# Optimization experiments

Hardware: AMD Instinct MI355X
Metric: run time of the kernel (lower is better)

The kernel has to match this reference:

```python
import jax, jax.numpy as jnp
import numpy as np
from jax import lax

EPS = 1e-5  # BatchNorm eps; eval-mode BN with running_mean=0, running_var=1


def _bn(v, g, b):
    return v * (g / jnp.sqrt(1.0 + EPS)) + b


def setup_inputs() -> dict:
    key = jax.random.key(0)
    ks = jax.random.split(key, 8)
    B, I, O, H, W, E, K, r = 16, 128, 128, 128, 128, 16, 3, 8
    Ir, Or = I // r, O // r
    f = jax.random.normal
    return {
        "x": f(ks[0], (B, I, H, W), jnp.float32),
        "experts": f(ks[1], (E, O, I, K, K), jnp.float32) * 0.05,
        "rw1": f(ks[2], (Ir, I), jnp.float32) * 0.05,
        "rbn1_g": jnp.ones((Ir,), jnp.float32),
        "rbn1_b": jnp.zeros((Ir,), jnp.float32),
        "rw2": f(ks[3], (I, Ir), jnp.float32) * 0.05,
        "rbn2_g": jnp.ones((I,), jnp.float32),
        "rbn2_b": jnp.zeros((I,), jnp.float32),
        "rw3": f(ks[4], (E, I), jnp.float32) * 0.05,
        "rb3": jnp.zeros((E,), jnp.float32),
        "ca_w1": f(ks[5], (Or, O), jnp.float32) * 0.05,
        "ca_bn1_g": jnp.ones((Or,), jnp.float32),
        "ca_bn1_b": jnp.zeros((Or,), jnp.float32),
        "ca_w2": f(ks[6], (O, Or), jnp.float32) * 0.05,
        "ca_bn2_g": jnp.ones((O,), jnp.float32),
        "ca_bn2_b": jnp.zeros((O,), jnp.float32),
        "sa_w": f(ks[7], (1, 2, 7, 7), jnp.float32) * 0.05,
        "sa_bn_g": jnp.ones((1,), jnp.float32),
        "sa_bn_b": jnp.zeros((1,), jnp.float32),
    }


def reference(x, experts, rw1, rbn1_g, rbn1_b, rw2, rbn2_g, rbn2_b, rw3, rb3,
              ca_w1, ca_bn1_g, ca_bn1_b, ca_w2, ca_bn2_g, ca_bn2_b,
              sa_w, sa_bn_g, sa_bn_b):
    B, I, H, W = x.shape
    E, O, _, K, _ = experts.shape
    # --- routing: avgpool -> 1x1 conv (matmul) -> BN -> ReLU -> 1x1 -> BN -> sigmoid -> 1x1 -> softmax
    p = jnp.mean(x, axis=(2, 3))                                  # [B, I]
    h = jax.nn.relu(_bn(p @ rw1.T, rbn1_g, rbn1_b))               # [B, I/r]
    g = jax.nn.sigmoid(_bn(h @ rw2.T, rbn2_g, rbn2_b))            # [B, I]
    rweights = jax.nn.softmax(g @ rw3.T + rb3, axis=1)            # [B, E]
    # --- expert-weighted kernel generation as a single GEMM
    w = jnp.einsum('be,eoihw->boihw', rweights, experts)          # [B, O, I, K, K]
    # --- per-sample conv via grouped conv (groups = B), stride=1, padding=1
    out = lax.conv_general_dilated(
        x.reshape(1, B * I, H, W),
        w.reshape(B * O, I, K, K),
        window_strides=(1, 1), padding=((1, 1), (1, 1)),
        dimension_numbers=('NCHW', 'OIHW', 'NCHW'),
        feature_group_count=B,
    ).reshape(B, O, H, W)
    # --- SE channel attention
    cp = jnp.mean(out, axis=(2, 3))                               # [B, O]
    ch = jax.nn.relu(_bn(cp @ ca_w1.T, ca_bn1_g, ca_bn1_b))
    cw = jax.nn.sigmoid(_bn(ch @ ca_w2.T, ca_bn2_g, ca_bn2_b))    # [B, O]
    out = out * cw[:, :, None, None]
    # --- CBAM spatial attention
    sp = jnp.concatenate([jnp.mean(out, axis=1, keepdims=True),
                          jnp.max(out, axis=1, keepdims=True)], axis=1)  # [B,2,H,W]
    sw = lax.conv_general_dilated(sp, sa_w, (1, 1), ((3, 3), (3, 3)),
                                  dimension_numbers=('NCHW', 'OIHW', 'NCHW'))
    sw = jax.nn.sigmoid(_bn(sw, sa_bn_g.reshape(1, 1, 1, 1), sa_bn_b.reshape(1, 1, 1, 1)))
    out = out * sw
    # --- residual (in_channels == out_channels -> Identity)
    return out + x
```

## Files before the change

### kernel.cpp

```cpp
#include <hip/hip_runtime.h>

typedef unsigned short ushort_t;
typedef __attribute__((ext_vector_type(4))) float float4_t;
typedef __attribute__((ext_vector_type(8))) short short8_t;
typedef __attribute__((ext_vector_type(8))) unsigned short ushort8_t;

__device__ __forceinline__ ushort_t f2bf(float f) {
    unsigned u = __builtin_bit_cast(unsigned, f);
    u = (u + 0x7fffu + ((u >> 16) & 1u)) >> 16;
    return (ushort_t)u;
}

__device__ __forceinline__ void gld16(const void* g, void* l) {
    __builtin_amdgcn_global_load_lds(
        (const __attribute__((address_space(1))) unsigned int*)g,
        (__attribute__((address_space(3))) unsigned int*)l, 16, 0, 0);
}


__global__ __launch_bounds__(256) void init_kernel(float* __restrict__ p, float* __restrict__ cp,
                                                   float* __restrict__ sp, ushort_t* __restrict__ xn) {
    int t = blockIdx.x * 256 + threadIdx.x;
    if (t < 2048) { p[t] = 0.f; return; }
    if (t < 4096) { cp[t - 2048] = 0.f; return; }
    if (t < 4096 + 574592) { sp[t - 4096] = 0.f; return; }
    int e = t - (4096 + 574592);
    if (e < 1056768) {
        int b = e / 66048;
        int r = e % 66048;
        int pix = r >> 7, i = r & 127;
        int hp, wp;
        if (pix < 130)      { hp = 0;   wp = pix; }
        else if (pix < 260) { hp = 129; wp = pix - 130; }
        else { int q = pix - 260; hp = 1 + (q >> 1); wp = (q & 1) ? 129 : 0; }
        xn[((b * 130 + hp) * 130 + wp) * 128 + i] = 0;
    }
}

__global__ __launch_bounds__(256) void transpose_kernel(const float* __restrict__ x,
                                                        ushort_t* __restrict__ xn,
                                                        float* __restrict__ p) {
    __shared__ float tile[128][65];
    int blk = blockIdx.x;
    int wt = blk & 1, h = (blk >> 1) & 127, b = blk >> 8;
    int w0 = wt * 64;
    int tid = threadIdx.x;
    int wl = tid & 63, ig = tid >> 6;
    const float* src = x + ((long)(b * 128) * 128 + h) * 128 + w0 + wl;
    #pragma unroll
    for (int i = ig; i < 128; i += 4) tile[i][wl] = src[(long)i * 16384];
    __syncthreads();
    if (tid < 128) {
        float s = 0.f;
        #pragma unroll
        for (int w = 0; w < 64; ++w) s += tile[tid][w];
        atomicAdd(&p[b * 128 + tid], s * (1.0f / 16384.0f));
    }
    int l16 = tid & 15, wq = tid >> 4;
    #pragma unroll
    for (int pass = 0; pass < 4; ++pass) {
        int w = wq + pass * 16;
        ushort8_t v;
        #pragma unroll
        for (int j = 0; j < 8; ++j) v[j] = f2bf(tile[l16 * 8 + j][w]);
        *(ushort8_t*)&xn[((b * 130 + h + 1) * 130 + (w0 + w + 1)) * 128 + l16 * 8] = v;
    }
}

__global__ __launch_bounds__(256) void routing_kernel(const float* __restrict__ p,
        const float* __restrict__ rw1, const float* __restrict__ g1, const float* __restrict__ b1,
        const float* __restrict__ rw2, const float* __restrict__ g2, const float* __restrict__ b2,
        const float* __restrict__ rw3, const float* __restrict__ rb3, float* __restrict__ rwt) {
    __shared__ float sh[16][16];
    __shared__ float sg[16][128];
    __shared__ float sl[16][16];
    int tid = threadIdx.x;
    const float bns = rsqrtf(1.0f + 1e-5f);
    {   int b = tid >> 4, j = tid & 15;
        float s = 0.f;
        for (int i = 0; i < 128; ++i) s += p[b * 128 + i] * rw1[j * 128 + i];
        s = s * (g1[j] * bns) + b1[j];
        sh[b][j] = fmaxf(s, 0.f); }
    __syncthreads();
    for (int c = 0; c < 8; ++c) {
        int idx = tid + c * 256;
        int b = idx >> 7, j = idx & 127;
        float s = 0.f;
        for (int k = 0; k < 16; ++k) s += sh[b][k] * rw2[j * 16 + k];
        s = s * (g2[j] * bns) + b2[j];
        sg[b][j] = 1.0f / (1.0f + expf(-s));
    }
    __syncthreads();
    {   int b = tid >> 4, e = tid & 15;
        float s = rb3[e];
        for (int j = 0; j < 128; ++j) s += sg[b][j] * rw3[e * 128 + j];
        sl[b][e] = s; }
    __syncthreads();
    {   int b = tid >> 4, e = tid & 15;
        float m = -1e30f;
        for (int k = 0; k < 16; ++k) m = fmaxf(m, sl[b][k]);
        float num = expf(sl[b][e] - m), den = 0.f;
        for (int k = 0; k < 16; ++k) den += expf(sl[b][k] - m);
        rwt[b * 16 + e] = num / den; }
}

__global__ __launch_bounds__(256) void wgen_kernel(const float* __restrict__ experts,
                                                   const float* __restrict__ rwt,
                                                   ushort_t* __restrict__ w2) {
    int b = blockIdx.x >> 7, o = blockIdx.x & 127;
    int tid = threadIdx.x;
    int i = tid & 127, eh = tid >> 7;
    __shared__ float rw[16];
    __shared__ float part[9][128];
    if (tid < 16) rw[tid] = rwt[b * 16 + tid];
    __syncthreads();
    float acc[9] = {0, 0, 0, 0, 0, 0, 0, 0, 0};
    const float* ep = experts + (long)(eh * 8) * 147456 + (o * 128 + i) * 9;
    #pragma unroll
    for (int e = 0; e < 8; ++e) {
        float r = rw[eh * 8 + e];
        const float* q = ep + (long)e * 147456;
        #pragma unroll
        for (int d = 0; d < 9; ++d) acc[d] += r * q[d];
    }
    if (eh) {
        #pragma unroll
        for (int d = 0; d < 9; ++d) part[d][i] = acc[d];
    }
    __syncthreads();
    if (!eh) {
        #pragma unroll
        for (int d = 0; d < 9; ++d)
            w2[((b * 9 + d) << 14) + (o << 7) + i] = f2bf(acc[d] + part[d][i]);
    }
}

struct __align__(16) ConvSmem {
    union {
        struct { ushort_t X[16640]; ushort_t A[2][4096]; } t;
        float c[4224];
    };
};

__global__ __launch_bounds__(256, 3) void conv_kernel(const ushort_t* __restrict__ xn,
                                                      const ushort_t* __restrict__ w2,
                                                      float* __restrict__ out,
                                                      float* __restrict__ cp) {
    __shared__ ConvSmem sm;
    int bh = blockIdx.x;
    int b = bh >> 7, h = bh & 127;
    int tid = threadIdx.x;
    int lane = tid & 63, wave = tid >> 6;
    int wm = wave & 1, wn = wave >> 1;
    int q = lane >> 4, nl = lane & 15;

    float4_t acc[4][4];
    #pragma unroll
    for (int mi = 0; mi < 4; ++mi)
        #pragma unroll
        for (int ni = 0; ni < 4; ++ni) acc[mi][ni] = (float4_t){0.f, 0.f, 0.f, 0.f};

    const ushort_t* xbase = xn + (b * 130 + h) * 16640;
    const ushort_t* abase = w2 + b * 9 * 16384;

    auto stageX = [&](int dy) {
        const ushort_t* xrow = xbase + dy * 16640;
        #pragma unroll
        for (int seg = wave; seg < 33; seg += 4) {
            if (seg < 32 || lane < 32) {
                int lofs = seg * 512 + lane * 8;
                int pp = lofs >> 7;
                int jb = (lofs & 127) >> 3;
                gld16(xrow + (pp << 7) + ((jb ^ (pp & 15)) << 3), &sm.t.X[seg * 512]);
            }
        }
    };
    auto stageA = [&](int dy, int dx, int ic, int buf) {
        const ushort_t* ab = abase + (dy * 3 + dx) * 16384 + ic * 32;
        int ol = lane >> 2;
        int jsrc = (lane & 3) ^ ((ol >> 1) & 3);
        #pragma unroll
        for (int inst = 0; inst < 2; ++inst) {
            int ob = wave * 32 + inst * 16;
            gld16(ab + (ob + ol) * 128 + (jsrc << 3), &sm.t.A[buf][ob * 32]);
        }
    };

    stageA(0, 0, 0, 0);
    stageX(0);

    #pragma unroll
    for (int dy = 0; dy < 3; ++dy) {
        if (dy > 0) { __syncthreads(); stageX(dy); }
        #pragma unroll
        for (int dx = 0; dx < 3; ++dx) {
            #pragma unroll
            for (int ic = 0; ic < 4; ++ic) {
                int c = (dy * 3 + dx) * 4 + ic;
                __syncthreads();
                if (c < 35) {
                    int cn = c + 1;
                    stageA(cn / 12, (cn % 12) >> 2, cn & 3, cn & 1);
                }
                int buf = c & 1;
                short8_t bfr[4], afr[4];
                #pragma unroll
                for (int ni = 0; ni < 4; ++ni) {
                    int pp = wn * 64 + ni * 16 + nl + dx;
                    int J = ic * 4 + q;
                    bfr[ni] = *(const short8_t*)&sm.t.X[(pp << 7) + ((J ^ (pp & 15)) << 3)];
                }
                #pragma unroll
                for (int mi = 0; mi < 4; ++mi) {
                    int o = wm * 64 + mi * 16 + nl;
                    afr[mi] = *(const short8_t*)&sm.t.A[buf][(o << 5) + ((q ^ ((o >> 1) & 3)) << 3)];
                }
                #pragma unroll
                for (int mi = 0; mi < 4; ++mi)
                    #pragma unroll
                    for (int ni = 0; ni < 4; ++ni)
                        acc[mi][ni] = __builtin_amdgcn_mfma_f32_16x16x32_bf16(
                            afr[mi], bfr[ni], acc[mi][ni], 0, 0, 0);
            }
        }
    }

    #pragma unroll
    for (int mi = 0; mi < 4; ++mi) {
        int o0 = wm * 64 + mi * 16 + q * 4;
        float rs[4] = {0.f, 0.f, 0.f, 0.f};
        #pragma unroll
        for (int ni = 0; ni < 4; ++ni) {
            float4_t v = acc[mi][ni];
            #pragma unroll
            for (int r = 0; r < 4; ++r) rs[r] += v[r];
        }
        #pragma unroll
        for (int r = 0; r < 4; ++r) {
            for (int msk = 1; msk < 16; msk <<= 1) rs[r] += __shfl_xor(rs[r], msk, 64);
            if (nl == 0) atomicAdd(&cp[(b << 7) + o0 + r], rs[r]);
        }
    }

    float* outb = out + (((long)(b << 7)) << 14) + (h << 7);
    #pragma unroll
    for (int os = 0; os < 4; ++os) {
        __syncthreads();
        if (wm == (os >> 1)) {
            #pragma unroll
            for (int mi2 = 0; mi2 < 2; ++mi2) {
                int mi = (os & 1) * 2 + mi2;
                #pragma unroll
                for (int ni = 0; ni < 4; ++ni) {
                    float4_t v = acc[mi][ni];
                    int orow = mi2 * 16 + q * 4;
                    int w = wn * 64 + ni * 16 + nl;
                    #pragma unroll
                    for (int rr = 0; rr < 4; ++rr) sm.c[(orow + rr) * 132 + w] = v[rr];
                }
            }
        }
        __syncthreads();
        int row = tid >> 3, j8 = tid & 7;
        float* og = outb + ((long)(os * 32 + row) << 14);
        #pragma unroll
        for (int k = 0; k < 4; ++k) {
            float4_t v = *(const float4_t*)&sm.c[row * 132 + j8 * 4 + k * 32];
            *(float4_t*)&og[j8 * 4 + k * 32] = v;
        }
    }
}

__global__ __launch_bounds__(256) void se_kernel(const float* __restrict__ cp,
        const float* __restrict__ w1, const float* __restrict__ g1, const float* __restrict__ b1,
        const float* __restrict__ w2, const float* __restrict__ g2, const float* __restrict__ b2,
        float* __restrict__ cw) {
    __shared__ float sc[16][128];
    __shared__ float sh[16][16];
    int tid = threadIdx.x;
    const float bns = rsqrtf(1.0f + 1e-5f);
    for (int c = 0; c < 8; ++c) {
        int idx = tid + c * 256;
        sc[idx >> 7][idx & 127] = cp[idx] * (1.0f / 16384.0f);
    }
    __syncthreads();
    {   int b = tid >> 4, j = tid & 15;
        float s = 0.f;
        for (int o = 0; o < 128; ++o) s += sc[b][o] * w1[j * 128 + o];
        s = s * (g1[j] * bns) + b1[j];
        sh[b][j] = fmaxf(s, 0.f); }
    __syncthreads();
    for (int c = 0; c < 8; ++c) {
        int idx = tid + c * 256;
        int b = idx >> 7, o = idx & 127;
        float s = 0.f;
        for (int k = 0; k < 16; ++k) s += sh[b][k] * w2[o * 16 + k];
        s = s * (g2[o] * bns) + b2[o];
        cw[idx] = 1.0f / (1.0f + expf(-s));
    }
}

__global__ __launch_bounds__(256) void stat_kernel(const float* __restrict__ out,
                                                   const float* __restrict__ cw,
                                                   float* __restrict__ sp) {
    int b = blockIdx.x >> 7, h = blockIdx.x & 127;
    int tid = threadIdx.x;
    int w = tid & 127, oh = tid >> 7;
    __shared__ float scw[128], ssum[128], smax[128];
    if (tid < 128) scw[tid] = cw[(b << 7) + tid];
    __syncthreads();
    const float* src = out + ((long)b << 21) + ((long)(oh * 64) << 14) + (h << 7) + w;
    float s = 0.f, m = -1e30f;
    #pragma unroll 8
    for (int o = 0; o < 64; ++o) {
        float v = src[(long)o << 14] * scw[oh * 64 + o];
        s += v;
        m = fmaxf(m, v);
    }
    if (oh) { ssum[w] = s; smax[w] = m; }
    __syncthreads();
    if (!oh) {
        s += ssum[w];
        m = fmaxf(m, smax[w]);
        float* d = sp + b * 2 * 17956;
        d[(h + 3) * 134 + (w + 3)] = s * (1.0f / 128.0f);
        d[17956 + (h + 3) * 134 + (w + 3)] = m;
    }
}

__global__ __launch_bounds__(128) void conv7_kernel(const float* __restrict__ sp,
        const float* __restrict__ k98, const float* __restrict__ g, const float* __restrict__ bb,
        float* __restrict__ sw) {
    int b = blockIdx.x >> 7, h = blockIdx.x & 127;
    int tid = threadIdx.x;
    __shared__ float ls[2][7][134];
    __shared__ float lk[98];
    const float* sb = sp + b * 2 * 17956;
    for (int idx = tid; idx < 2 * 7 * 134; idx += 128) {
        int c = idx / 938, rr = idx % 938;
        int ky = rr / 134, wp = rr % 134;
        ls[c][ky][wp] = sb[c * 17956 + (h + ky) * 134 + wp];
    }
    if (tid < 98) lk[tid] = k98[tid];
    __syncthreads();
    float s = 0.f;
    #pragma unroll
    for (int c = 0; c < 2; ++c)
        #pragma unroll
        for (int ky = 0; ky < 7; ++ky)
            #pragma unroll
            for (int kx = 0; kx < 7; ++kx)
                s += ls[c][ky][tid + kx] * lk[c * 49 + ky * 7 + kx];
    s = s * (g[0] * rsqrtf(1.0f + 1e-5f)) + bb[0];
    sw[(blockIdx.x << 7) + tid] = 1.0f / (1.0f + expf(-s));
}

__global__ __launch_bounds__(256) void final_kernel(float* __restrict__ out,
        const float* __restrict__ x, const float* __restrict__ cw, const float* __restrict__ sw) {
    int t = blockIdx.x * 256 + threadIdx.x;
    int w4 = t & 31, h = (t >> 5) & 127, o = (t >> 12) & 127, b = t >> 19;
    float c = cw[(b << 7) + o];
    int idx = (((b << 7) + o) << 14) + (h << 7) + (w4 << 2);
    float4_t ov = *(const float4_t*)&out[idx];
    float4_t xv = *(const float4_t*)&x[idx];
    float4_t sv = *(const float4_t*)&sw[(((b << 7) + h) << 7) + (w4 << 2)];
    float4_t r = ov * c * sv + xv;
    *(float4_t*)&out[idx] = r;
}

extern "C" void kernel_launch(void* const* d_in, const int* in_sizes, int n_in,
                              void* d_out, int out_size, void* d_ws, size_t ws_size,
                              hipStream_t stream) {
    const float* x       = (const float*)d_in[0];
    const float* experts = (const float*)d_in[1];
    const float* rw1     = (const float*)d_in[2];
    const float* rbn1_g  = (const float*)d_in[3];
    const float* rbn1_b  = (const float*)d_in[4];
    const float* rw2     = (const float*)d_in[5];
    const float* rbn2_g  = (const float*)d_in[6];
    const float* rbn2_b  = (const float*)d_in[7];
    const float* rw3     = (const float*)d_in[8];
    const float* rb3     = (const float*)d_in[9];
    const float* ca_w1   = (const float*)d_in[10];
    const float* ca_bn1g = (const float*)d_in[11];
    const float* ca_bn1b = (const float*)d_in[12];
    const float* ca_w2   = (const float*)d_in[13];
    const float* ca_bn2g = (const float*)d_in[14];
    const float* ca_bn2b = (const float*)d_in[15];
    const float* sa_w    = (const float*)d_in[16];
    const float* sa_g    = (const float*)d_in[17];
    const float* sa_b    = (const float*)d_in[18];
    float* out = (float*)d_out;
    char* ws = (char*)d_ws;

    ushort_t* xn  = (ushort_t*)(ws);
    ushort_t* w2  = (ushort_t*)(ws + 69222400);
    float*    p   = (float*)(ws + 73940992);
    float*    cp  = (float*)(ws + 73949184);
    float*    rwt = (float*)(ws + 73957376);
    float*    cw  = (float*)(ws + 73958400);
    float*    sp  = (float*)(ws + 73966592);
    float*    sw  = (float*)(ws + 76264960);

    hipLaunchKernelGGL(init_kernel, dim3(6389), dim3(256), 0, stream, p, cp, sp, xn);
    hipLaunchKernelGGL(transpose_kernel, dim3(4096), dim3(256), 0, stream, x, xn, p);
    hipLaunchKernelGGL(routing_kernel, dim3(1), dim3(256), 0, stream,
                       p, rw1, rbn1_g, rbn1_b, rw2, rbn2_g, rbn2_b, rw3, rb3, rwt);
    hipLaunchKernelGGL(wgen_kernel, dim3(2048), dim3(256), 0, stream, experts, rwt, w2);
    hipLaunchKernelGGL(conv_kernel, dim3(2048), dim3(256), 0, stream, xn, w2, out, cp);
    hipLaunchKernelGGL(se_kernel, dim3(1), dim3(256), 0, stream,
                       cp, ca_w1, ca_bn1g, ca_bn1b, ca_w2, ca_bn2g, ca_bn2b, cw);
    hipLaunchKernelGGL(stat_kernel, dim3(2048), dim3(256), 0, stream, out, cw, sp);
    hipLaunchKernelGGL(conv7_kernel, dim3(2048), dim3(128), 0, stream, sp, sa_w, sa_g, sa_b, sw);
    hipLaunchKernelGGL(final_kernel, dim3(32768), dim3(256), 0, stream, out, x, cw, sw);
}
```

Before: 537.6 us.

## Load conv weight fragments directly from global, remap blocks, fuse spatial attention with final

The conv kernel no longer stages per-tap weight tiles through double-buffered LDS. Each lane now reads its A fragments straight from global memory, which drops most of the per-chunk barriers and frees LDS so occupancy can rise to 4 blocks per CU. Block indices are remapped so that concurrently running blocks come from different samples, which changes cache locality for the weights and activations. The 7x7 spatial-attention conv is fused with the final scale-and-residual pass, removing the sw buffer round trip and one kernel launch. The cost is higher global/L2 latency on the weight fragment loads, which are now synchronous with the MFMA inner loop.

Result: slower. 597.1 us (+11.1%).

```diff
diff --git a/kernel.cpp b/kernel.cpp
--- a/kernel.cpp
+++ b/kernel.cpp
@@ -137,17 +137,17 @@
 
 struct __align__(16) ConvSmem {
     union {
-        struct { ushort_t X[16640]; ushort_t A[2][4096]; } t;
+        ushort_t X[16640];
         float c[4224];
     };
 };
 
-__global__ __launch_bounds__(256, 3) void conv_kernel(const ushort_t* __restrict__ xn,
+__global__ __launch_bounds__(256, 4) void conv_kernel(const ushort_t* __restrict__ xn,
                                                       const ushort_t* __restrict__ w2,
                                                       float* __restrict__ out,
                                                       float* __restrict__ cp) {
     __shared__ ConvSmem sm;
-    int bh = blockIdx.x;
+    int bh = (blockIdx.x & 7) * 256 + (blockIdx.x >> 3);
     int b = bh >> 7, h = bh & 127;
     int tid = threadIdx.x;
     int lane = tid & 63, wave = tid >> 6;
@@ -161,7 +161,7 @@
         for (int ni = 0; ni < 4; ++ni) acc[mi][ni] = (float4_t){0.f, 0.f, 0.f, 0.f};
 
     const ushort_t* xbase = xn + (b * 130 + h) * 16640;
-    const ushort_t* abase = w2 + b * 9 * 16384;
+    const ushort_t* abase = w2 + (long)b * 147456 + (wm * 64 + nl) * 128 + q * 8;
 
     auto stageX = [&](int dy) {
         const ushort_t* xrow = xbase + dy * 16640;
@@ -171,49 +171,31 @@
                 int lofs = seg * 512 + lane * 8;
                 int pp = lofs >> 7;
                 int jb = (lofs & 127) >> 3;
-                gld16(xrow + (pp << 7) + ((jb ^ (pp & 15)) << 3), &sm.t.X[seg * 512]);
+                gld16(xrow + (pp << 7) + ((jb ^ (pp & 15)) << 3), &sm.X[seg * 512]);
             }
         }
     };
-    auto stageA = [&](int dy, int dx, int ic, int buf) {
-        const ushort_t* ab = abase + (dy * 3 + dx) * 16384 + ic * 32;
-        int ol = lane >> 2;
-        int jsrc = (lane & 3) ^ ((ol >> 1) & 3);
-        #pragma unroll
-        for (int inst = 0; inst < 2; ++inst) {
-            int ob = wave * 32 + inst * 16;
-            gld16(ab + (ob + ol) * 128 + (jsrc << 3), &sm.t.A[buf][ob * 32]);
-        }
-    };
-
-    stageA(0, 0, 0, 0);
-    stageX(0);
 
     #pragma unroll
     for (int dy = 0; dy < 3; ++dy) {
-        if (dy > 0) { __syncthreads(); stageX(dy); }
+        if (dy) __syncthreads();
+        stageX(dy);
+        asm volatile("s_waitcnt vmcnt(0)" ::: "memory");
+        __syncthreads();
         #pragma unroll
         for (int dx = 0; dx < 3; ++dx) {
+            const ushort_t* ap = abase + (dy * 3 + dx) * 16384;
             #pragma unroll
             for (int ic = 0; ic < 4; ++ic) {
-                int c = (dy * 3 + dx) * 4 + ic;
-                __syncthreads();
-                if (c < 35) {
-                    int cn = c + 1;
-                    stageA(cn / 12, (cn % 12) >> 2, cn & 3, cn & 1);
-                }
-                int buf = c & 1;
-                short8_t bfr[4], afr[4];
+                short8_t afr[4], bfr[4];
+                #pragma unroll
+                for (int mi = 0; mi < 4; ++mi)
+                    afr[mi] = *(const short8_t*)&ap[mi * 2048 + ic * 32];
                 #pragma unroll
                 for (int ni = 0; ni < 4; ++ni) {
                     int pp = wn * 64 + ni * 16 + nl + dx;
                     int J = ic * 4 + q;
-                    bfr[ni] = *(const short8_t*)&sm.t.X[(pp << 7) + ((J ^ (pp & 15)) << 3)];
-                }
-                #pragma unroll
-                for (int mi = 0; mi < 4; ++mi) {
-                    int o = wm * 64 + mi * 16 + nl;
-                    afr[mi] = *(const short8_t*)&sm.t.A[buf][(o << 5) + ((q ^ ((o >> 1) & 3)) << 3)];
+                    bfr[ni] = *(const short8_t*)&sm.X[(pp << 7) + ((J ^ (pp & 15)) << 3)];
                 }
                 #pragma unroll
                 for (int mi = 0; mi < 4; ++mi)
@@ -328,44 +310,48 @@
     }
 }
 
-__global__ __launch_bounds__(128) void conv7_kernel(const float* __restrict__ sp,
+__global__ __launch_bounds__(256) void sattn_kernel(const float* __restrict__ sp,
         const float* __restrict__ k98, const float* __restrict__ g, const float* __restrict__ bb,
-        float* __restrict__ sw) {
+        const float* __restrict__ cw, const float* __restrict__ x, float* __restrict__ out) {
     int b = blockIdx.x >> 7, h = blockIdx.x & 127;
     int tid = threadIdx.x;
     __shared__ float ls[2][7][134];
     __shared__ float lk[98];
+    __shared__ float sws[128];
+    __shared__ float scw[128];
     const float* sb = sp + b * 2 * 17956;
-    for (int idx = tid; idx < 2 * 7 * 134; idx += 128) {
+    for (int idx = tid; idx < 2 * 7 * 134; idx += 256) {
         int c = idx / 938, rr = idx % 938;
         int ky = rr / 134, wp = rr % 134;
         ls[c][ky][wp] = sb[c * 17956 + (h + ky) * 134 + wp];
     }
     if (tid < 98) lk[tid] = k98[tid];
-    __syncthreads();
-    float s = 0.f;
-    #pragma unroll
-    for (int c = 0; c < 2; ++c)
-        #pragma unroll
-        for (int ky = 0; ky < 7; ++ky)
+    if (tid >= 128) scw[tid - 128] = cw[(b << 7) + (tid - 128)];
+    __syncthreads();
+    if (tid < 128) {
+        float s = 0.f;
+        #pragma unroll
+        for (int c = 0; c < 2; ++c)
             #pragma unroll
-            for (int kx = 0; kx < 7; ++kx)
-                s += ls[c][ky][tid + kx] * lk[c * 49 + ky * 7 + kx];
-    s = s * (g[0] * rsqrtf(1.0f + 1e-5f)) + bb[0];
-    sw[(blockIdx.x << 7) + tid] = 1.0f / (1.0f + expf(-s));
-}
-
-__global__ __launch_bounds__(256) void final_kernel(float* __restrict__ out,
-        const float* __restrict__ x, const float* __restrict__ cw, const float* __restrict__ sw) {
-    int t = blockIdx.x * 256 + threadIdx.x;
-    int w4 = t & 31, h = (t >> 5) & 127, o = (t >> 12) & 127, b = t >> 19;
-    float c = cw[(b << 7) + o];
-    int idx = (((b << 7) + o) << 14) + (h << 7) + (w4 << 2);
-    float4_t ov = *(const float4_t*)&out[idx];
-    float4_t xv = *(const float4_t*)&x[idx];
-    float4_t sv = *(const float4_t*)&sw[(((b << 7) + h) << 7) + (w4 << 2)];
-    float4_t r = ov * c * sv + xv;
-    *(float4_t*)&out[idx] = r;
+            for (int ky = 0; ky < 7; ++ky)
+                #pragma unroll
+                for (int kx = 0; kx < 7; ++kx)
+                    s += ls[c][ky][tid + kx] * lk[c * 49 + ky * 7 + kx];
+        s = s * (g[0] * rsqrtf(1.0f + 1e-5f)) + bb[0];
+        sws[tid] = 1.0f / (1.0f + expf(-s));
+    }
+    __syncthreads();
+    int w4 = tid & 31, og = tid >> 5;
+    long base = (((long)b << 21) + (h << 7)) + (w4 << 2);
+    float4_t sv = *(const float4_t*)&sws[w4 << 2];
+    #pragma unroll
+    for (int o = og; o < 128; o += 8) {
+        long idx = base + ((long)o << 14);
+        float4_t ov = *(const float4_t*)&out[idx];
+        float4_t xv = *(const float4_t*)&x[idx];
+        float4_t r = ov * scw[o] * sv + xv;
+        *(float4_t*)&out[idx] = r;
+    }
 }
 
 extern "C" void kernel_launch(void* const* d_in, const int* in_sizes, int n_in,
@@ -400,7 +386,6 @@
     float*    rwt = (float*)(ws + 73957376);
     float*    cw  = (float*)(ws + 73958400);
     float*    sp  = (float*)(ws + 73966592);
-    float*    sw  = (float*)(ws + 76264960);
 
     hipLaunchKernelGGL(init_kernel, dim3(6389), dim3(256), 0, stream, p, cp, sp, xn);
     hipLaunchKernelGGL(transpose_kernel, dim3(4096), dim3(256), 0, stream, x, xn, p);
@@ -411,6 +396,6 @@
     hipLaunchKernelGGL(se_kernel, dim3(1), dim3(256), 0, stream,
                        cp, ca_w1, ca_bn1g, ca_bn1b, ca_w2, ca_bn2g, ca_bn2b, cw);
     hipLaunchKernelGGL(stat_kernel, dim3(2048), dim3(256), 0, stream, out, cw, sp);
-    hipLaunchKernelGGL(conv7_kernel, dim3(2048), dim3(128), 0, stream, sp, sa_w, sa_g, sa_b, sw);
-    hipLaunchKernelGGL(final_kernel, dim3(32768), dim3(256), 0, stream, out, x, cw, sw);
-}
+    hipLaunchKernelGGL(sattn_kernel, dim3(2048), dim3(256), 0, stream,
+                       sp, sa_w, sa_g, sa_b, cw, x, out);
+}
```
